# Performance work log

Measured on AMD Instinct MI355X. Metric: run time of the kernel, lower is better.

Reference implementation:

```python
import jax, jax.numpy as jnp
import jax.scipy.linalg as jsp
import numpy as np

# Problem dimensions (match init_kwargs P_shape/A_shape)
N = 256   # variables
M = 512   # constraints
B = 64    # batch

# OSQP ADMM hyper-parameters (fixed-rho variant of the OSQP algorithm)
SIGMA = 1e-6
RHO = 0.1
ALPHA = 1.6
N_ITERS = 500


def setup_inputs() -> dict:
    key = jax.random.key(0)
    kP, kq, kA, kc = jax.random.split(key, 4)
    # P is diagonal with strictly positive entries -> PSD (values are the nnz of P)
    P_val = jax.random.uniform(kP, (B, N), dtype=jnp.float32) + 0.1
    q_val = jax.random.normal(kq, (B, N), dtype=jnp.float32)
    # A is a dense pattern; values stored row-major as its nnz vector
    A_val = jax.random.normal(kA, (B, M * N), dtype=jnp.float32) / np.sqrt(N)
    # Feasible box: l <= u by construction
    center = jax.random.normal(kc, (B, M), dtype=jnp.float32)
    l_val = center - 1.0
    u_val = center + 1.0
    return {"P_val": P_val, "q_val": q_val, "A_val": A_val, "l_val": l_val, "u_val": u_val}


def _admm_qp(P_val, q_val, A_val, l_val, u_val):
    """Batched OSQP-style ADMM solve of min 1/2 x'Px + q'x  s.t. l <= Ax <= u.

    P is diagonal (nnz pattern = diag), A is dense (nnz pattern = full m x n).
    """
    A = A_val.reshape(B, M, N)                      # [B,m,n]
    # KKT-like matrix M_k = P + sigma*I + rho*A'A   [B,n,n]
    eye = jnp.eye(N, dtype=P_val.dtype)
    P_diag = P_val + SIGMA                          # diagonal of P + sigma*I
    Mk = RHO * jnp.einsum('bmi,bmj->bij', A, A) + jax.vmap(jnp.diag)(P_diag)
    L = jnp.linalg.cholesky(Mk)                     # [B,n,n], factor once, reuse
    Lt = jnp.swapaxes(L, -1, -2)

    def kkt_solve(rhs):                             # rhs [B,n]
        y1 = jsp.solve_triangular(L, rhs[..., None], lower=True)
        y2 = jsp.solve_triangular(Lt, y1, lower=False)
        return y2[..., 0]

    x0 = jnp.zeros((B, N), dtype=P_val.dtype)
    z0 = jnp.zeros((B, M), dtype=P_val.dtype)
    y0 = jnp.zeros((B, M), dtype=P_val.dtype)

    def step(state, _):
        x, z, y = state
        rhs = SIGMA * x - q_val + jnp.einsum('bmn,bm->bn', A, RHO * z - y)
        x_t = kkt_solve(rhs)                        # x-tilde
        z_t = jnp.einsum('bmn,bn->bm', A, x_t)      # z-tilde = A x_t
        x_new = ALPHA * x_t + (1.0 - ALPHA) * x
        z_hat = ALPHA * z_t + (1.0 - ALPHA) * z
        z_new = jnp.clip(z_hat + y / RHO, l_val, u_val)
        y_new = y + RHO * (z_hat - z_new)
        return (x_new, z_new, y_new), None

    (x, _, _), _ = jax.lax.scan(step, (x0, z0, y0), None, length=N_ITERS)
    return x


def reference(P_val, q_val, A_val, l_val, u_val):
    return _admm_qp(P_val, q_val, A_val, l_val, u_val)   # [B, n] primal solutions
```

## Files before the change

### kernel.cpp

```cpp
#include <hip/hip_runtime.h>
#include <hip/hip_fp16.h>

#define N_VAR 256
#define M_CON 512
#define BATCH 64
#define SIGMA_C 1e-6f
#define RHO_C 0.1f
#define ALPHA_C 1.6f
#define NITERS 500

typedef _Float16 f16x8 __attribute__((ext_vector_type(8)));
typedef float f32x4 __attribute__((ext_vector_type(4)));

__global__ __launch_bounds__(256) void k_transpose(const float* __restrict__ A,
                                                   float* __restrict__ At) {
  __shared__ float tile[32][33];
  int b = blockIdx.z;
  int n0 = blockIdx.x * 32;
  int m0 = blockIdx.y * 32;
  const float* Ab = A + (size_t)b * (M_CON * N_VAR);
  float* Atb = At + (size_t)b * (M_CON * N_VAR);
  int tx = threadIdx.x, ty = threadIdx.y;
#pragma unroll
  for (int j = 0; j < 32; j += 8)
    tile[ty + j][tx] = Ab[(size_t)(m0 + ty + j) * N_VAR + n0 + tx];
  __syncthreads();
#pragma unroll
  for (int j = 0; j < 32; j += 8)
    Atb[(size_t)(n0 + ty + j) * M_CON + m0 + tx] = tile[tx][ty + j];
}

__global__ __launch_bounds__(256) void k_cast_split(
    const float* __restrict__ in, unsigned* __restrict__ oh,
    unsigned* __restrict__ oe, int n4) {
  int i = blockIdx.x * 256 + threadIdx.x;
  if (i >= n4) return;
  float4 v = ((const float4*)in)[i];
  __half2 h01 = __floats2half2_rn(v.x, v.y);
  __half2 h23 = __floats2half2_rn(v.z, v.w);
  float2 f01 = __half22float2(h01);
  float2 f23 = __half22float2(h23);
  __half2 e01 = __floats2half2_rn((v.x - f01.x) * 256.0f, (v.y - f01.y) * 256.0f);
  __half2 e23 = __floats2half2_rn((v.z - f23.x) * 256.0f, (v.w - f23.y) * 256.0f);
  uint2 uh; uh.x = *(unsigned*)&h01; uh.y = *(unsigned*)&h23;
  uint2 ue; ue.x = *(unsigned*)&e01; ue.y = *(unsigned*)&e23;
  ((uint2*)oh)[i] = uh;
  ((uint2*)oe)[i] = ue;
}

__global__ __launch_bounds__(256, 4) void k_mfma_nt(
    const _Float16* __restrict__ Xh, const _Float16* __restrict__ Xe,
    const _Float16* __restrict__ Yh, const _Float16* __restrict__ Ye,
    float* __restrict__ C0, float* __restrict__ C1,
    int K, int jTiles, long long bsX, long long bsY, long long bsC,
    float alpha, const float* __restrict__ diagv, int mode) {
  int b = blockIdx.y;
  int bx = blockIdx.x;
  int t = threadIdx.x, l = t & 63, wv = t >> 6;
  int i0 = (bx / jTiles) * 32;
  int j0 = (bx % jTiles) * 128 + wv * 32;
  const _Float16* Xhb = Xh + (size_t)b * bsX;
  const _Float16* Xeb = Xe + (size_t)b * bsX;
  const _Float16* Yhb = Yh + (size_t)b * bsY;
  const _Float16* Yeb = Ye + (size_t)b * bsY;

  int lr = l & 15, lk = (l >> 4) * 8;
  f32x4 m00 = {0,0,0,0}, m01 = {0,0,0,0}, m10 = {0,0,0,0}, m11 = {0,0,0,0};
  f32x4 c00 = {0,0,0,0}, c01 = {0,0,0,0}, c10 = {0,0,0,0}, c11 = {0,0,0,0};
  f32x4 s00 = {0,0,0,0}, s01 = {0,0,0,0}, s10 = {0,0,0,0}, s11 = {0,0,0,0};

  for (int kk = 0; kk < K; kk += 32) {
    f16x8 xh0 = *(const f16x8*)&Xhb[(size_t)(i0 + lr) * K + kk + lk];
    f16x8 xh1 = *(const f16x8*)&Xhb[(size_t)(i0 + 16 + lr) * K + kk + lk];
    f16x8 xe0 = *(const f16x8*)&Xeb[(size_t)(i0 + lr) * K + kk + lk];
    f16x8 xe1 = *(const f16x8*)&Xeb[(size_t)(i0 + 16 + lr) * K + kk + lk];
    f16x8 yh0 = *(const f16x8*)&Yhb[(size_t)(j0 + lr) * K + kk + lk];
    f16x8 yh1 = *(const f16x8*)&Yhb[(size_t)(j0 + 16 + lr) * K + kk + lk];
    f16x8 ye0 = *(const f16x8*)&Yeb[(size_t)(j0 + lr) * K + kk + lk];
    f16x8 ye1 = *(const f16x8*)&Yeb[(size_t)(j0 + 16 + lr) * K + kk + lk];
    m00 = __builtin_amdgcn_mfma_f32_16x16x32_f16(xh0, yh0, m00, 0, 0, 0);
    m01 = __builtin_amdgcn_mfma_f32_16x16x32_f16(xh0, yh1, m01, 0, 0, 0);
    m10 = __builtin_amdgcn_mfma_f32_16x16x32_f16(xh1, yh0, m10, 0, 0, 0);
    m11 = __builtin_amdgcn_mfma_f32_16x16x32_f16(xh1, yh1, m11, 0, 0, 0);
    c00 = __builtin_amdgcn_mfma_f32_16x16x32_f16(xh0, ye0, c00, 0, 0, 0);
    c01 = __builtin_amdgcn_mfma_f32_16x16x32_f16(xh0, ye1, c01, 0, 0, 0);
    c10 = __builtin_amdgcn_mfma_f32_16x16x32_f16(xh1, ye0, c10, 0, 0, 0);
    c11 = __builtin_amdgcn_mfma_f32_16x16x32_f16(xh1, ye1, c11, 0, 0, 0);
    c00 = __builtin_amdgcn_mfma_f32_16x16x32_f16(xe0, yh0, c00, 0, 0, 0);
    c01 = __builtin_amdgcn_mfma_f32_16x16x32_f16(xe0, yh1, c01, 0, 0, 0);
    c10 = __builtin_amdgcn_mfma_f32_16x16x32_f16(xe1, yh0, c10, 0, 0, 0);
    c11 = __builtin_amdgcn_mfma_f32_16x16x32_f16(xe1, yh1, c11, 0, 0, 0);
    s00 = __builtin_amdgcn_mfma_f32_16x16x32_f16(xe0, ye0, s00, 0, 0, 0);
    s01 = __builtin_amdgcn_mfma_f32_16x16x32_f16(xe0, ye1, s01, 0, 0, 0);
    s10 = __builtin_amdgcn_mfma_f32_16x16x32_f16(xe1, ye0, s10, 0, 0, 0);
    s11 = __builtin_amdgcn_mfma_f32_16x16x32_f16(xe1, ye1, s11, 0, 0, 0);
  }

#pragma unroll
  for (int tr = 0; tr < 2; ++tr)
#pragma unroll
    for (int tc = 0; tc < 2; ++tc) {
      f32x4 vm = tr ? (tc ? m11 : m10) : (tc ? m01 : m00);
      f32x4 vc = tr ? (tc ? c11 : c10) : (tc ? c01 : c00);
      f32x4 vs = tr ? (tc ? s11 : s10) : (tc ? s01 : s00);
#pragma unroll
      for (int r = 0; r < 4; ++r) {
        float v = (vm[r] + vc[r] * (1.0f / 256.0f) +
                   vs[r] * (1.0f / 65536.0f)) * alpha;
        int gi = i0 + tr * 16 + (l >> 4) * 4 + r;
        int gj = j0 + tc * 16 + lr;
        if (mode == 0) {
          if (diagv != nullptr && gi == gj)
            v += diagv[(size_t)b * N_VAR + gi] + SIGMA_C;
          C0[(size_t)b * bsC + (size_t)gi * 256 + gj] = v;
        } else {
          _Float16 fh = (_Float16)v;
          _Float16 fe = (_Float16)((v - (float)fh) * 256.0f);
          ((_Float16*)C0)[(size_t)b * bsC + (size_t)gi * 256 + gj] = fh;
          ((_Float16*)C1)[(size_t)b * bsC + (size_t)gi * 256 + gj] = fe;
        }
      }
    }
}

__global__ __launch_bounds__(256, 4) void k_mfma_g(
    const _Float16* __restrict__ Fh, const _Float16* __restrict__ Fe,
    const _Float16* __restrict__ Ah, const _Float16* __restrict__ Ae,
    unsigned* __restrict__ Gp) {
  int b = blockIdx.y;
  int bx = blockIdx.x;
  int t = threadIdx.x, l = t & 63, wv = t >> 6;
  int i0 = (bx >> 2) * 32;
  int j0 = (bx & 3) * 128 + wv * 32;
  const _Float16* Fhb = Fh + (size_t)b * 131072;
  const _Float16* Feb = Fe + (size_t)b * 131072;
  const _Float16* Ahb = Ah + (size_t)b * 131072;
  const _Float16* Aeb = Ae + (size_t)b * 131072;
  unsigned* Gpb = Gp + (size_t)b * 131072;

  int lr = l & 15, lk = (l >> 4) * 8;
  f32x4 acc00 = {0,0,0,0}, acc01 = {0,0,0,0}, acc10 = {0,0,0,0}, acc11 = {0,0,0,0};
  f32x4 ar00 = {0,0,0,0}, ar01 = {0,0,0,0}, ar10 = {0,0,0,0}, ar11 = {0,0,0,0};

  for (int kk = 0; kk < 256; kk += 32) {
    f16x8 af0 = *(const f16x8*)&Fhb[(size_t)(i0 + lr) * 256 + kk + lk];
    f16x8 af1 = *(const f16x8*)&Fhb[(size_t)(i0 + 16 + lr) * 256 + kk + lk];
    f16x8 ae0 = *(const f16x8*)&Feb[(size_t)(i0 + lr) * 256 + kk + lk];
    f16x8 ae1 = *(const f16x8*)&Feb[(size_t)(i0 + 16 + lr) * 256 + kk + lk];
    f16x8 bf0 = *(const f16x8*)&Ahb[(size_t)(j0 + lr) * 256 + kk + lk];
    f16x8 bf1 = *(const f16x8*)&Ahb[(size_t)(j0 + 16 + lr) * 256 + kk + lk];
    f16x8 be0 = *(const f16x8*)&Aeb[(size_t)(j0 + lr) * 256 + kk + lk];
    f16x8 be1 = *(const f16x8*)&Aeb[(size_t)(j0 + 16 + lr) * 256 + kk + lk];
    acc00 = __builtin_amdgcn_mfma_f32_16x16x32_f16(af0, bf0, acc00, 0, 0, 0);
    acc01 = __builtin_amdgcn_mfma_f32_16x16x32_f16(af0, bf1, acc01, 0, 0, 0);
    acc10 = __builtin_amdgcn_mfma_f32_16x16x32_f16(af1, bf0, acc10, 0, 0, 0);
    acc11 = __builtin_amdgcn_mfma_f32_16x16x32_f16(af1, bf1, acc11, 0, 0, 0);
    ar00 = __builtin_amdgcn_mfma_f32_16x16x32_f16(af0, be0, ar00, 0, 0, 0);
    ar01 = __builtin_amdgcn_mfma_f32_16x16x32_f16(af0, be1, ar01, 0, 0, 0);
    ar10 = __builtin_amdgcn_mfma_f32_16x16x32_f16(af1, be0, ar10, 0, 0, 0);
    ar11 = __builtin_amdgcn_mfma_f32_16x16x32_f16(af1, be1, ar11, 0, 0, 0);
    ar00 = __builtin_amdgcn_mfma_f32_16x16x32_f16(ae0, bf0, ar00, 0, 0, 0);
    ar01 = __builtin_amdgcn_mfma_f32_16x16x32_f16(ae0, bf1, ar01, 0, 0, 0);
    ar10 = __builtin_amdgcn_mfma_f32_16x16x32_f16(ae1, bf0, ar10, 0, 0, 0);
    ar11 = __builtin_amdgcn_mfma_f32_16x16x32_f16(ae1, bf1, ar11, 0, 0, 0);
  }

#pragma unroll
  for (int tr = 0; tr < 2; ++tr)
#pragma unroll
    for (int tc = 0; tc < 2; ++tc) {
      const f32x4* am = (tr == 0) ? ((tc == 0) ? &acc00 : &acc01)
                                  : ((tc == 0) ? &acc10 : &acc11);
      const f32x4* ae = (tr == 0) ? ((tc == 0) ? &ar00 : &ar01)
                                  : ((tc == 0) ? &ar10 : &ar11);
#pragma unroll
      for (int r = 0; r < 4; ++r) {
        float v = (*am)[r] + (*ae)[r] * (1.0f / 256.0f);
        float vp = __shfl_xor(v, 1);
        int gi = i0 + tr * 16 + (l >> 4) * 4 + r;
        int gj = j0 + tc * 16 + lr;
        if (!(l & 1)) {
          __half2 hh = __floats2half2_rn(v, vp);
          int sl = gi >> 7, rl = gi & 127;
          int t2 = ((((gj >> 7) << 1) | (rl >> 6)) << 6) | (rl & 63);
          Gpb[(size_t)sl * 32768 + ((gj & 127) >> 1) * 512 + t2] = *(unsigned*)&hh;
        }
      }
    }
}

__global__ __launch_bounds__(512, 2) void k_invert(const float* __restrict__ Mk,
                                                   float* __restrict__ Mi) {
  int b = blockIdx.x;
  const float* src = Mk + (size_t)b * 65536;
  float* dst = Mi + (size_t)b * 65536;
  int t = threadIdx.x;
  int c = t & 255, rh = t >> 8;

  float a[128];
#pragma unroll
  for (int j = 0; j < 128; ++j) a[j] = src[(size_t)(rh * 128 + j) * 256 + c];

  __shared__ float colPan[256][8];
  __shared__ float rowPan[2][8][260];
  __shared__ float PiSh[64];
  __shared__ float Rp[8][260];

  int rh_s = __builtin_amdgcn_readfirstlane(rh);
  int cw_s = __builtin_amdgcn_readfirstlane((t >> 6) & 3);

  if (rh == 0) {
#pragma unroll
    for (int j = 0; j < 8; ++j) rowPan[0][j][c] = a[j];
  }
  __syncthreads();

  for (int s = 0; s < 32; ++s) {
    int kb = s * 8;
    int cur = s & 1, nxt = cur ^ 1;
    int kh = kb >> 7, kj = kb & 127;
    int khn = (kb + 8) >> 7, kjn = (kb + 8) & 127;
    bool mycol = (c >= kb) && (c < kb + 8);

    if (cw_s == (kb >> 6)) {
      if (mycol) {
        int f = c - kb;
#pragma unroll
        for (int j = 0; j < 128; ++j) colPan[rh * 128 + j][f] = a[j];
      }
    }
    if (t < 64) {
      int e = t >> 3, f = t & 7;
      float p = rowPan[cur][e][kb + f];
#pragma unroll
      for (int k2 = 0; k2 < 8; ++k2) {
        float piv = __shfl(p, k2 * 8 + k2);
        float rv = __shfl(p, k2 * 8 + f);
        float cv = __shfl(p, e * 8 + k2);
        float pivinv = 1.0f / piv;
        float srv = rv * pivinv;
        float gen = p - cv * srv;
        p = gen;
        if (e == k2) p = srv;
        if (f == k2) p = -cv * pivinv;
        if (e == k2 && f == k2) p = pivinv;
      }
      PiSh[t] = p;
    }
    __syncthreads();

    float rpan[8];
#pragma unroll
    for (int f2 = 0; f2 < 8; ++f2) rpan[f2] = rowPan[cur][f2][c];
    float rp[8];
#pragma unroll
    for (int e = 0; e < 8; ++e) {
      float4 p0 = *(const float4*)&PiSh[e * 8];
      float4 p1 = *(const float4*)&PiSh[e * 8 + 4];
      rp[e] = p0.x * rpan[0] + p0.y * rpan[1] + p0.z * rpan[2] + p0.w * rpan[3] +
              p1.x * rpan[4] + p1.y * rpan[5] + p1.z * rpan[6] + p1.w * rpan[7];
    }
    if (cw_s == (kb >> 6)) {
      if (mycol) {
        int f = c - kb;
#pragma unroll
        for (int e = 0; e < 8; ++e) rp[e] = PiSh[e * 8 + f];
      }
    }
#pragma unroll
    for (int e = 0; e < 8; ++e) Rp[e][c] = rp[e];

    bool myhalfk = (rh_s == kh);
    bool stashw = (s != 31) && (rh_s == khn);
#pragma unroll
    for (int j = 0; j < 128; ++j) {
      float4 c0 = *(const float4*)&colPan[rh * 128 + j][0];
      float4 c1 = *(const float4*)&colPan[rh * 128 + j][4];
      float aold = a[j];
      float nv = aold -
                 (c0.x * rp[0] + c0.y * rp[1] + c0.z * rp[2] + c0.w * rp[3] +
                  c1.x * rp[4] + c1.y * rp[5] + c1.z * rp[6] + c1.w * rp[7]);
      if (mycol) nv -= aold;
      if (myhalfk && j >= kj && j < kj + 8)
        nv = Rp[j - kj][c];
      a[j] = nv;
      if (stashw && j >= kjn && j < kjn + 8)
        rowPan[nxt][j - kjn][c] = nv;
    }
    __syncthreads();
  }

#pragma unroll
  for (int j = 0; j < 128; ++j) dst[(size_t)(rh * 128 + j) * 256 + c] = a[j];
}

__global__ __launch_bounds__(256) void k_matvec_h(const float* __restrict__ Mi,
                                                  const float* __restrict__ q,
                                                  float* __restrict__ h) {
  int b = blockIdx.x, t = threadIdx.x;
  __shared__ float qs[256];
  qs[t] = q[(size_t)b * 256 + t];
  __syncthreads();
  const float* Mb = Mi + (size_t)b * 65536;
  float acc = 0.0f;
  for (int k = 0; k < 256; ++k) acc += Mb[(size_t)k * 256 + t] * qs[k];
  h[(size_t)b * 256 + t] = acc;
}

__global__ __launch_bounds__(512) void k_matvec_d(const float* __restrict__ At,
                                                  const float* __restrict__ h,
                                                  float* __restrict__ d) {
  int b = blockIdx.x, t = threadIdx.x;
  __shared__ float hs[256];
  if (t < 256) hs[t] = h[(size_t)b * 256 + t];
  __syncthreads();
  const float* Ab = At + (size_t)b * 131072;
  float acc = 0.0f;
  for (int n = 0; n < 256; ++n) acc += Ab[(size_t)n * 512 + t] * hs[n];
  d[(size_t)b * 512 + t] = acc;
}

__global__ __launch_bounds__(512) void k_admm4(
    const unsigned* __restrict__ Gpk_g, const float* __restrict__ dvec,
    const float* __restrict__ lv, const float* __restrict__ uv,
    unsigned long long* __restrict__ wtag, float* __restrict__ Sbuf) {
  int g = blockIdx.x;
  int b = (g & 7) + 8 * ((g >> 3) & 7);
  int s = g >> 6;
  int t = threadIdx.x;
  int l = t & 63, wv = t >> 6;
  int c0 = wv * 64;
  int cg = wv >> 1, hc = wv & 1;

  __shared__ __align__(16) float wbuf[8][64];
  __shared__ float part[2][8][128];

  const unsigned* gsrc =
      Gpk_g + (size_t)(b * 4 + s) * 32768 + (size_t)(hc * 32) * 512 + cg * 128 + l;

  float zreg = 0.0f, yreg = 0.0f, Sreg = 0.0f;
  float lreg = 0.0f, ureg = 0.0f, dreg = 0.0f;
  if (t < 128) {
    lreg = lv[(size_t)b * 512 + s * 128 + t];
    ureg = uv[(size_t)b * 512 + s * 128 + t];
    dreg = dvec[(size_t)b * 512 + s * 128 + t];
  }
  wbuf[wv][l] = 0.0f;

  unsigned long long* wt0 = wtag + (size_t)b * 512;
  unsigned long long* wt1 = wtag + 32768 + (size_t)b * 512;
  const float4* wq4 = (const float4*)(wbuf[wv]);

  for (int it = 0; it < NITERS; ++it) {
    if (it > 0) {
      unsigned long long* wp = (it & 1) ? wt1 : wt0;
      unsigned want = (unsigned)it;
      unsigned long long v = __hip_atomic_load(&wp[c0 + l], __ATOMIC_RELAXED,
                                               __HIP_MEMORY_SCOPE_AGENT);
      bool got = ((unsigned)(v >> 32) == want);
      while (!__all(got)) {
        if (!got) {
          unsigned long long v2 = __hip_atomic_load(
              &wp[c0 + l], __ATOMIC_RELAXED, __HIP_MEMORY_SCOPE_AGENT);
          if ((unsigned)(v2 >> 32) == want) { v = v2; got = true; }
        }
      }
      wbuf[wv][l] = __uint_as_float((unsigned)(v & 0xffffffffu));
    }

    float r0a = 0.f, r0b = 0.f, r1a = 0.f, r1b = 0.f;
#pragma unroll
    for (int j = 0; j < 8; ++j) {
      float4 wa = wq4[2 * j];
      float4 wc = wq4[2 * j + 1];
      unsigned a0 = gsrc[(4 * j + 0) * 512];
      unsigned a1 = gsrc[(4 * j + 1) * 512];
      unsigned a2 = gsrc[(4 * j + 2) * 512];
      unsigned a3 = gsrc[(4 * j + 3) * 512];
      unsigned b0 = gsrc[(4 * j + 0) * 512 + 64];
      unsigned b1 = gsrc[(4 * j + 1) * 512 + 64];
      unsigned b2 = gsrc[(4 * j + 2) * 512 + 64];
      unsigned b3 = gsrc[(4 * j + 3) * 512 + 64];
      float2 fa0 = __half22float2(*(__half2*)&a0);
      float2 fa1 = __half22float2(*(__half2*)&a1);
      float2 fa2 = __half22float2(*(__half2*)&a2);
      float2 fa3 = __half22float2(*(__half2*)&a3);
      float2 fb0 = __half22float2(*(__half2*)&b0);
      float2 fb1 = __half22float2(*(__half2*)&b1);
      float2 fb2 = __half22float2(*(__half2*)&b2);
      float2 fb3 = __half22float2(*(__half2*)&b3);
      r0a += fa0.x * wa.x + fa0.y * wa.y + fa1.x * wa.z + fa1.y * wa.w;
      r0b += fa2.x * wc.x + fa2.y * wc.y + fa3.x * wc.z + fa3.y * wc.w;
      r1a += fb0.x * wa.x + fb0.y * wa.y + fb1.x * wa.z + fb1.y * wa.w;
      r1b += fb2.x * wc.x + fb2.y * wc.y + fb3.x * wc.z + fb3.y * wc.w;
    }
    int pp = it & 1;
    part[pp][wv][l] = r0a + r0b;
    part[pp][wv][64 + l] = r1a + r1b;
    __syncthreads();

    if (t < 128) {
      float w_old = RHO_C * zreg - yreg;
      Sreg = w_old - 0.6f * Sreg;
      float p = part[pp][0][t] + part[pp][1][t] + part[pp][2][t] +
                part[pp][3][t] + part[pp][4][t] + part[pp][5][t] +
                part[pp][6][t] + part[pp][7][t];
      float zt = p - dreg;
      float zh = ALPHA_C * zt + (1.0f - ALPHA_C) * zreg;
      float zc = zh + yreg * (1.0f / RHO_C);
      zc = fminf(fmaxf(zc, lreg), ureg);
      yreg += RHO_C * (zh - zc);
      zreg = zc;
      if (it < NITERS - 1) {
        float wn = RHO_C * zreg - yreg;
        unsigned long long pk =
            ((unsigned long long)(unsigned)(it + 1) << 32) |
            (unsigned long long)__float_as_uint(wn);
        unsigned long long* wp = ((it + 1) & 1) ? wt1 : wt0;
        __hip_atomic_store(&wp[s * 128 + t], pk, __ATOMIC_RELAXED,
                           __HIP_MEMORY_SCOPE_AGENT);
      }
    }
  }

  if (t < 128) Sbuf[(size_t)b * 512 + s * 128 + t] = Sreg;
}

__global__ __launch_bounds__(256) void k_final(
    const float* __restrict__ A, const float* __restrict__ q,
    const float* __restrict__ Mi, const float* __restrict__ Sbuf,
    float* __restrict__ xout) {
  int b = blockIdx.x, t = threadIdx.x;
  __shared__ float Ssh[512];
  __shared__ float uu[256];
  for (int i = t; i < 512; i += 256) Ssh[i] = Sbuf[(size_t)b * 512 + i];
  __syncthreads();
  const float* Ab = A + (size_t)b * 131072;
  float acc = 0.0f;
  for (int m = 0; m < 512; ++m) acc += Ab[(size_t)m * 256 + t] * Ssh[m];
  uu[t] = ALPHA_C * acc - q[(size_t)b * 256 + t];
  __syncthreads();
  const float* Mb = Mi + (size_t)b * 65536;
  float x = 0.0f;
  for (int kk = 0; kk < 256; ++kk) x += Mb[(size_t)kk * 256 + t] * uu[kk];
  xout[(size_t)b * 256 + t] = x;
}

extern "C" void kernel_launch(void* const* d_in, const int* in_sizes, int n_in,
                              void* d_out, int out_size, void* d_ws, size_t ws_size,
                              hipStream_t stream) {
  (void)in_sizes; (void)n_in; (void)out_size; (void)ws_size;
  const float* P = (const float*)d_in[0];
  const float* q = (const float*)d_in[1];
  const float* Av = (const float*)d_in[2];
  const float* lv = (const float*)d_in[3];
  const float* uv = (const float*)d_in[4];
  float* xout = (float*)d_out;

  float* ws = (float*)d_ws;
  float* At = ws;
  float* Fh = ws;
  float* Fe = ws + 4194304;
  float* Mi = ws + 8388608;
  float* Mk = ws + 12582912;
  unsigned* Mih = (unsigned*)(ws + 12582912);
  unsigned* Mie = (unsigned*)(ws + 14680064);
  unsigned* Gp = (unsigned*)(ws + 12582912);
  unsigned* Ath = (unsigned*)(ws + 20971520);
  unsigned* Ate = (unsigned*)(ws + 25165824);
  unsigned* Ah = (unsigned*)(ws + 20971520);
  unsigned* Ae = (unsigned*)(ws + 25165824);
  float* hv = ws + 29360128;
  float* dv = ws + 29376512;
  float* Sbuf = ws + 29409280;
  unsigned long long* wtag = (unsigned long long*)(ws + 29442048);

  hipMemsetAsync(wtag, 0, 524288, stream);

  k_transpose<<<dim3(8, 16, 64), dim3(32, 8), 0, stream>>>(Av, At);
  k_cast_split<<<8192, 256, 0, stream>>>(At, Ath, Ate, 2097152);
  k_mfma_nt<<<dim3(16, 64), 256, 0, stream>>>(
      (const _Float16*)Ath, (const _Float16*)Ate,
      (const _Float16*)Ath, (const _Float16*)Ate,
      Mk, nullptr, 512, 2, 131072LL, 131072LL, 65536LL, RHO_C, P, 0);
  k_invert<<<64, 512, 0, stream>>>(Mk, Mi);
  k_matvec_h<<<64, 256, 0, stream>>>(Mi, q, hv);
  k_matvec_d<<<64, 512, 0, stream>>>(At, hv, dv);
  k_cast_split<<<8192, 256, 0, stream>>>(Av, Ah, Ae, 2097152);
  k_cast_split<<<4096, 256, 0, stream>>>(Mi, Mih, Mie, 1048576);
  k_mfma_nt<<<dim3(32, 64), 256, 0, stream>>>(
      (const _Float16*)Ah, (const _Float16*)Ae,
      (const _Float16*)Mih, (const _Float16*)Mie,
      Fh, Fe, 256, 2, 131072LL, 65536LL, 131072LL, 1.0f, nullptr, 1);
  k_mfma_g<<<dim3(64, 64), 256, 0, stream>>>(
      (const _Float16*)Fh, (const _Float16*)Fe,
      (const _Float16*)Ah, (const _Float16*)Ae, Gp);
  k_admm4<<<256, 512, 0, stream>>>(Gp, dv, lv, uv, wtag, Sbuf);
  k_final<<<64, 256, 0, stream>>>(Av, q, Mi, Sbuf, xout);
}
```

Baseline: 1.557 ms.

## Keep per-thread G slice resident in LDS and registers across ADMM iterations

The G matrix producer now writes a thread-major layout so each admm thread owns 64 contiguous words. The ADMM kernel loads that slice once: 13 uint4 go into shared memory (about 104KB) and 3 uint4 are pinned in registers. Before, every iteration re-read G from global memory or L2. This removes per-iteration global traffic from the 500-iteration loop, at the cost of heavy LDS use that limits occupancy to one block per CU.

```diff
diff --git a/kernel.cpp b/kernel.cpp
--- a/kernel.cpp
+++ b/kernel.cpp
@@ -126,7 +126,7 @@
 __global__ __launch_bounds__(256, 4) void k_mfma_g(
     const _Float16* __restrict__ Fh, const _Float16* __restrict__ Fe,
     const _Float16* __restrict__ Ah, const _Float16* __restrict__ Ae,
-    unsigned* __restrict__ Gp) {
+    unsigned* __restrict__ Gt) {
   int b = blockIdx.y;
   int bx = blockIdx.x;
   int t = threadIdx.x, l = t & 63, wv = t >> 6;
@@ -136,7 +136,6 @@
   const _Float16* Feb = Fe + (size_t)b * 131072;
   const _Float16* Ahb = Ah + (size_t)b * 131072;
   const _Float16* Aeb = Ae + (size_t)b * 131072;
-  unsigned* Gpb = Gp + (size_t)b * 131072;
 
   int lr = l & 15, lk = (l >> 4) * 8;
   f32x4 acc00 = {0,0,0,0}, acc01 = {0,0,0,0}, acc10 = {0,0,0,0}, acc11 = {0,0,0,0};
@@ -182,8 +181,9 @@
         if (!(l & 1)) {
           __half2 hh = __floats2half2_rn(v, vp);
           int sl = gi >> 7, rl = gi & 127;
-          int t2 = ((((gj >> 7) << 1) | (rl >> 6)) << 6) | (rl & 63);
-          Gpb[(size_t)sl * 32768 + ((gj & 127) >> 1) * 512 + t2] = *(unsigned*)&hh;
+          int thr = (gj >> 6) * 64 + (rl & 63);
+          int kword = (rl >> 6) * 32 + ((gj & 63) >> 1);
+          Gt[((size_t)(b * 4 + sl) * 512 + thr) * 64 + kword] = *(unsigned*)&hh;
         }
       }
     }
@@ -321,7 +321,7 @@
 }
 
 __global__ __launch_bounds__(512) void k_admm4(
-    const unsigned* __restrict__ Gpk_g, const float* __restrict__ dvec,
+    const unsigned* __restrict__ Gt, const float* __restrict__ dvec,
     const float* __restrict__ lv, const float* __restrict__ uv,
     unsigned long long* __restrict__ wtag, float* __restrict__ Sbuf) {
   int g = blockIdx.x;
@@ -330,13 +330,18 @@
   int t = threadIdx.x;
   int l = t & 63, wv = t >> 6;
   int c0 = wv * 64;
-  int cg = wv >> 1, hc = wv & 1;
-
+
+  __shared__ __align__(16) uint4 GsV[13 * 512];
   __shared__ __align__(16) float wbuf[8][64];
   __shared__ float part[2][8][128];
 
-  const unsigned* gsrc =
-      Gpk_g + (size_t)(b * 4 + s) * 32768 + (size_t)(hc * 32) * 512 + cg * 128 + l;
+  const uint4* gsrc = (const uint4*)(Gt + ((size_t)(b * 4 + s) * 512 + t) * 64);
+#pragma unroll
+  for (int k = 0; k < 13; ++k) GsV[k * 512 + t] = gsrc[k];
+  uint4 r13 = gsrc[13], r14 = gsrc[14], r15 = gsrc[15];
+  asm volatile("" : "+v"(r13.x), "+v"(r13.y), "+v"(r13.z), "+v"(r13.w));
+  asm volatile("" : "+v"(r14.x), "+v"(r14.y), "+v"(r14.z), "+v"(r14.w));
+  asm volatile("" : "+v"(r15.x), "+v"(r15.y), "+v"(r15.z), "+v"(r15.w));
 
   float zreg = 0.0f, yreg = 0.0f, Sreg = 0.0f;
   float lreg = 0.0f, ureg = 0.0f, dreg = 0.0f;
@@ -373,22 +378,20 @@
     for (int j = 0; j < 8; ++j) {
       float4 wa = wq4[2 * j];
       float4 wc = wq4[2 * j + 1];
-      unsigned a0 = gsrc[(4 * j + 0) * 512];
-      unsigned a1 = gsrc[(4 * j + 1) * 512];
-      unsigned a2 = gsrc[(4 * j + 2) * 512];
-      unsigned a3 = gsrc[(4 * j + 3) * 512];
-      unsigned b0 = gsrc[(4 * j + 0) * 512 + 64];
-      unsigned b1 = gsrc[(4 * j + 1) * 512 + 64];
-      unsigned b2 = gsrc[(4 * j + 2) * 512 + 64];
-      unsigned b3 = gsrc[(4 * j + 3) * 512 + 64];
-      float2 fa0 = __half22float2(*(__half2*)&a0);
-      float2 fa1 = __half22float2(*(__half2*)&a1);
-      float2 fa2 = __half22float2(*(__half2*)&a2);
-      float2 fa3 = __half22float2(*(__half2*)&a3);
-      float2 fb0 = __half22float2(*(__half2*)&b0);
-      float2 fb1 = __half22float2(*(__half2*)&b1);
-      float2 fb2 = __half22float2(*(__half2*)&b2);
-      float2 fb3 = __half22float2(*(__half2*)&b3);
+      uint4 ga = GsV[j * 512 + t];
+      uint4 gb;
+      if (j < 5)      gb = GsV[(8 + j) * 512 + t];
+      else if (j == 5) gb = r13;
+      else if (j == 6) gb = r14;
+      else             gb = r15;
+      float2 fa0 = __half22float2(*(__half2*)&ga.x);
+      float2 fa1 = __half22float2(*(__half2*)&ga.y);
+      float2 fa2 = __half22float2(*(__half2*)&ga.z);
+      float2 fa3 = __half22float2(*(__half2*)&ga.w);
+      float2 fb0 = __half22float2(*(__half2*)&gb.x);
+      float2 fb1 = __half22float2(*(__half2*)&gb.y);
+      float2 fb2 = __half22float2(*(__half2*)&gb.z);
+      float2 fb3 = __half22float2(*(__half2*)&gb.w);
       r0a += fa0.x * wa.x + fa0.y * wa.y + fa1.x * wa.z + fa1.y * wa.w;
       r0b += fa2.x * wc.x + fa2.y * wc.y + fa3.x * wc.z + fa3.y * wc.w;
       r1a += fb0.x * wa.x + fb0.y * wa.y + fb1.x * wa.z + fb1.y * wa.w;
@@ -465,7 +468,7 @@
   float* Mk = ws + 12582912;
   unsigned* Mih = (unsigned*)(ws + 12582912);
   unsigned* Mie = (unsigned*)(ws + 14680064);
-  unsigned* Gp = (unsigned*)(ws + 12582912);
+  unsigned* Gt = (unsigned*)(ws + 12582912);
   unsigned* Ath = (unsigned*)(ws + 20971520);
   unsigned* Ate = (unsigned*)(ws + 25165824);
   unsigned* Ah = (unsigned*)(ws + 20971520);
@@ -494,7 +497,7 @@
       Fh, Fe, 256, 2, 131072LL, 65536LL, 131072LL, 1.0f, nullptr, 1);
   k_mfma_g<<<dim3(64, 64), 256, 0, stream>>>(
       (const _Float16*)Fh, (const _Float16*)Fe,
-      (const _Float16*)Ah, (const _Float16*)Ae, Gp);
-  k_admm4<<<256, 512, 0, stream>>>(Gp, dv, lv, uv, wtag, Sbuf);
+      (const _Float16*)Ah, (const _Float16*)Ae, Gt);
+  k_admm4<<<256, 512, 0, stream>>>(Gt, dv, lv, uv, wtag, Sbuf);
   k_final<<<64, 256, 0, stream>>>(Av, q, Mi, Sbuf, xout);
 }
```

Result: slower. 1.706 ms (+9.6%).
